# Kernel tuning notes

Hardware: AMD Instinct MI355X
Metric: run time of the kernel (lower is better)

Reference implementation:

```python
import jax, jax.numpy as jnp
import numpy as np
import math

D_MODEL = 1024
N_HEADS = 16
D_K = D_MODEL // N_HEADS
B, S = 4, 1024
MAX_REL = 64  # table built for 2*64-1 positions, clamped beyond


def setup_inputs() -> dict:
    key = jax.random.key(0)
    ks = jax.random.split(key, 11)
    init = 1.0 / math.sqrt(D_MODEL)
    def lin(k):
        kw, kb = jax.random.split(k)
        W = jax.random.uniform(kw, (D_MODEL, D_MODEL), jnp.float32, -init, init)
        b = jax.random.uniform(kb, (D_MODEL,), jnp.float32, -init, init)
        return W, b
    wq, bq = lin(ks[0]); wk, bk = lin(ks[1]); wv, bv = lin(ks[2]); wo, bo = lin(ks[3])
    x = jax.random.normal(ks[4], (B, S, D_MODEL), jnp.float32)
    rel_table = jax.random.normal(ks[5], (2 * MAX_REL - 1, N_HEADS), jnp.float32)
    mask = jnp.ones((B, 1, 1, S), jnp.int32)
    return {"x": x, "mask": mask, "wq": wq, "bq": bq, "wk": wk, "bk": bk,
            "wv": wv, "bv": bv, "wo": wo, "bo": bo, "rel_table": rel_table}


def reference(x, mask, wq, bq, wk, bk, wv, bv, wo, bo, rel_table):
    Bn, Sn, Dm = x.shape
    scale = math.sqrt(D_K)
    def heads(y):  # [B,S,D] -> [B,H,S,dk]
        return y.reshape(Bn, Sn, N_HEADS, D_K).transpose(0, 2, 1, 3)
    Q = heads(x @ wq.T + bq)
    K = heads(x @ wk.T + bk)
    V = heads(x @ wv.T + bv)
    scores = jnp.einsum('bhqd,bhkd->bhqk', Q, K) / scale
    # relative position bias gather, clamped to table range
    rel = jnp.arange(Sn)[None, :] - jnp.arange(Sn)[:, None] + MAX_REL - 1
    rel = jnp.clip(rel, 0, 2 * MAX_REL - 2)
    bias = rel_table[rel]                      # [S,S,H]
    scores = scores + bias.transpose(2, 0, 1)[None]  # [B,H,S,S]
    scores = jnp.where(mask == 0, jnp.float32(-1e9), scores)
    attn = jax.nn.softmax(scores, axis=-1)
    ctx = jnp.einsum('bhqk,bhkd->bhqd', attn, V)
    ctx = ctx.transpose(0, 2, 1, 3).reshape(Bn, Sn, Dm)
    return ctx @ wo.T + bo
```

## Files before the change

kernel.cpp:

```cpp
#include <hip/hip_runtime.h>
#include <hip/hip_bf16.h>

typedef __attribute__((ext_vector_type(8))) short short8;
typedef __attribute__((ext_vector_type(4))) short short4v;
typedef __attribute__((ext_vector_type(4))) float f32x4;

#define D_MODEL 1024
#define N_HEADS 16
#define D_KK 64
#define BATCH 4
#define SEQ 1024
#define NTOK (BATCH*SEQ)

#define LOG2E  1.44269504f
#define SCALE2 (0.125f * 1.44269504f)
#define NEGBIG (-1.44269504e9f)

#if __has_builtin(__builtin_amdgcn_mfma_f32_16x16x16bf16_1k)
#define HAVE_MFMA16 1
#else
#define HAVE_MFMA16 0
#endif

#if __has_builtin(__builtin_amdgcn_exp2f)
#define EXP2(x) __builtin_amdgcn_exp2f(x)
#else
#define EXP2(x) exp2f(x)
#endif

template<int N> struct ic { static constexpr int value = N; };

__device__ __forceinline__ short f2b(float f){
  unsigned u = __float_as_uint(f);
  u += 0x7fffu + ((u >> 16) & 1u);
  return (short)(u >> 16);
}

__device__ __forceinline__ void gl2lds16(const void* g, void* l){
  __builtin_amdgcn_global_load_lds(
      (const __attribute__((address_space(1))) void*)g,
      (__attribute__((address_space(3))) void*)l, 16, 0, 0);
}

__device__ __forceinline__ float max3f(float a, float b, float c){
  float d; asm("v_max3_f32 %0, %1, %2, %3" : "=v"(d) : "v"(a), "v"(b), "v"(c)); return d;
}
__device__ __forceinline__ float tmax16(const f32x4* sc){
  float t = max3f(sc[0][0], sc[0][1], sc[0][2]);
  t = max3f(t, sc[0][3], sc[1][0]);
  t = max3f(t, sc[1][1], sc[1][2]);
  t = max3f(t, sc[1][3], sc[2][0]);
  t = max3f(t, sc[2][1], sc[2][2]);
  t = max3f(t, sc[2][3], sc[3][0]);
  t = max3f(t, sc[3][1], sc[3][2]);
  return fmaxf(t, sc[3][3]);
}

__global__ __launch_bounds__(256) void cvt_all_kernel(
    const float* __restrict__ x,  const float* __restrict__ wq,
    const float* __restrict__ wk, const float* __restrict__ wv,
    const float* __restrict__ wo, short* __restrict__ dst)
{
  const size_t NX = (size_t)NTOK * D_MODEL;
  const size_t NW = (size_t)D_MODEL * D_MODEL;
  size_t e = ((size_t)blockIdx.x * 256 + threadIdx.x) * 4;
  const float* s;
  size_t off;
  if      (e < NX)        { s = x;  off = e; }
  else if (e < NX +   NW) { s = wq; off = e - NX; }
  else if (e < NX + 2*NW) { s = wk; off = e - NX -   NW; }
  else if (e < NX + 3*NW) { s = wv; off = e - NX - 2*NW; }
  else                    { s = wo; off = e - NX - 3*NW; }
  f32x4 v = *reinterpret_cast<const f32x4*>(s + off);
  short4v o;
  o[0]=f2b(v[0]); o[1]=f2b(v[1]); o[2]=f2b(v[2]); o[3]=f2b(v[3]);
  *reinterpret_cast<short4v*>(dst + e) = o;
}

template<int BN, int MODE, bool PRESC>
__device__ __forceinline__ void gemm_bt_body(const short* __restrict__ A,
    const short* __restrict__ W, const float* __restrict__ bias,
    void* __restrict__ Cout, int N, int K, int bm0, int bn0,
    short* AsB, short* BsB)
{
  constexpr int NF = BN / 32;
  const int tid = threadIdx.x, lane = tid & 63, w = tid >> 6;
  const int wr = w >> 1, wc = w & 1;
  const int srow = lane >> 3;
  const int scol = ((lane & 7) ^ srow) * 8;
  const int fr = lane & 15, g = lane >> 4;

  f32x4 acc[4][NF];
  #pragma unroll
  for (int m=0;m<4;m++)
    #pragma unroll
    for (int n=0;n<NF;n++) acc[m][n] = (f32x4){0.f,0.f,0.f,0.f};

  for (int k0 = 0; k0 < K; k0 += 64){
    __syncthreads();
    #pragma unroll
    for (int i=0;i<4;i++){
      const int c = w*4 + i;
      gl2lds16(A + (size_t)(bm0 + c*8 + srow)*K + k0 + scol, &AsB[c*8*64]);
    }
    #pragma unroll
    for (int i=0;i<NF;i++){
      const int c = w*NF + i;
      gl2lds16(W + (size_t)(bn0 + c*8 + srow)*K + k0 + scol, &BsB[c*8*64]);
    }
    __syncthreads();
    #pragma unroll
    for (int f=0; f<2; f++){
      short8 af[4], bfr[NF];
      #pragma unroll
      for (int m=0;m<4;m++){
        const int rr = wr*64 + m*16 + fr;
        af[m] = *reinterpret_cast<const short8*>(
            (const char*)AsB + rr*128 + ((g*16 + f*64) ^ ((rr&7)<<4)));
      }
      #pragma unroll
      for (int n=0;n<NF;n++){
        const int rr = wc*(BN/2) + n*16 + fr;
        bfr[n] = *reinterpret_cast<const short8*>(
            (const char*)BsB + rr*128 + ((g*16 + f*64) ^ ((rr&7)<<4)));
      }
      #pragma unroll
      for (int m=0;m<4;m++)
        #pragma unroll
        for (int n=0;n<NF;n++)
          acc[m][n] = __builtin_amdgcn_mfma_f32_16x16x32_bf16(af[m], bfr[n], acc[m][n], 0,0,0);
    }
  }

  #pragma unroll
  for (int n=0;n<NF;n++){
    const int col = bn0 + wc*(BN/2) + n*16 + fr;
    const float bv = bias[col];
    if (MODE == 2){
      const int hh = col >> 6, dd = col & 63;
      #pragma unroll
      for (int m=0;m<4;m++){
        const int row0 = bm0 + wr*64 + m*16 + g*4;
        const int bb = row0 >> 10, ss = row0 & 1023;
        short4v o;
        #pragma unroll
        for (int r=0;r<4;r++){
          float v = acc[m][n][r] + bv;
          if (PRESC) v *= SCALE2;
          o[r] = f2b(v);
        }
        *reinterpret_cast<short4v*>(
            (short*)Cout + ((size_t)(bb*N_HEADS+hh)*D_KK + dd)*SEQ + ss) = o;
      }
    } else {
      #pragma unroll
      for (int m=0;m<4;m++){
        const int row0 = bm0 + wr*64 + m*16 + g*4;
        #pragma unroll
        for (int r=0;r<4;r++){
          float v = acc[m][n][r] + bv;
          if (PRESC) v *= SCALE2;
          if (MODE == 1) ((float*)Cout)[(size_t)(row0+r)*N + col] = v;
          else           ((short*)Cout)[(size_t)(row0+r)*N + col] = f2b(v);
        }
      }
    }
  }
}

__global__ __launch_bounds__(256) void qkv_gemm_kernel(
    const short* __restrict__ X,
    const short* __restrict__ Wq, const short* __restrict__ Wk, const short* __restrict__ Wv,
    const float* __restrict__ bq, const float* __restrict__ bk, const float* __restrict__ bv,
    short* __restrict__ Q, short* __restrict__ K, short* __restrict__ V)
{
  __shared__ short As[128*64];
  __shared__ short Bs[64*64];
  const int bid = blockIdx.x;
  const int xcd = bid & 7, s = bid >> 3;
  const int z = s >> 6;
  const int rem = s & 63;
  const int bn0 = (rem >> 2) * 64;
  const int bm0 = (xcd * 4 + (rem & 3)) * 128;
  if (z == 0)      gemm_bt_body<64,0,true >(X, Wq, bq, Q, D_MODEL, D_MODEL, bm0, bn0, As, Bs);
  else if (z == 1) gemm_bt_body<64,0,false>(X, Wk, bk, K, D_MODEL, D_MODEL, bm0, bn0, As, Bs);
  else             gemm_bt_body<64,2,false>(X, Wv, bv, V, D_MODEL, D_MODEL, bm0, bn0, As, Bs);
}

__global__ __launch_bounds__(256) void out_gemm_kernel(
    const short* __restrict__ Ctx, const short* __restrict__ Wo,
    const float* __restrict__ bo, float* __restrict__ Out)
{
  __shared__ short As[128*64];
  __shared__ short Bs[64*64];
  const int bid = blockIdx.x;
  const int xcd = bid & 7, s = bid >> 3;
  const int bn0 = (s >> 2) * 64;
  const int bm0 = (xcd * 4 + (s & 3)) * 128;
  gemm_bt_body<64,1,false>(Ctx, Wo, bo, Out, D_MODEL, D_MODEL, bm0, bn0, As, Bs);
}

__global__ __launch_bounds__(512, 2) void attn_kernel(
    const short* __restrict__ Qb, const short* __restrict__ Kb,
    const short* __restrict__ Vtg, const int* __restrict__ mask,
    const float* __restrict__ rel_table, short* __restrict__ Ctx)
{
  const int bid = blockIdx.x;
  const int xcd = bid & 7, slot = bid >> 3;
  const int bh = xcd * 8 + (slot >> 3);
  const int qt = slot & 7;
  const int b = bh >> 4, h = bh & 15;
  const int q0 = qt * 128;
  const int tid = threadIdx.x, lane = tid & 63, w = tid >> 6;
  const int team = w >> 2, wt = w & 3;
  const int fr = lane & 15, g = lane >> 4;

  __shared__ short kvbuf[2][2][2][64][64];
  __shared__ float rel_pad[384];
  __shared__ float mb_all[2][8][64];
  __shared__ float ml[128][2];

  for (int i = tid; i < 384; i += 512){
    int d = i - 128;
    d = d < 0 ? 0 : (d > 126 ? 126 : d);
    rel_pad[i] = rel_table[d * N_HEADS + h] * LOG2E;
  }
  const float cb_lo = rel_table[0*N_HEADS + h]   * LOG2E;
  const float cb_hi = rel_table[126*N_HEADS + h] * LOG2E;

  for (int e = tid; e < 1024; e += 512){
    const int tm = e >> 9, tt = (e >> 6) & 7, i = e & 63;
    const int kvt = tm*512 + tt*64;
    const int delta = kvt - q0;
    const bool far = (delta <= -128 || delta >= 192);
    const float cb = far ? (delta > 0 ? cb_hi : cb_lo) : 0.f;
    mb_all[tm][tt][i] = mask[b*SEQ + kvt + i] ? cb : NEGBIG;
  }

  const short* Qg = Qb + (size_t)b*SEQ*D_MODEL + h*D_KK;
  const short* Kg = Kb + (size_t)b*SEQ*D_MODEL + h*D_KK;
  const short* Vg = Vtg + (size_t)bh*D_KK*SEQ;

  const int qa = q0 + wt*32 + fr;
  const int qb = qa + 16;
  short8 qfa[2], qfb[2];
  #pragma unroll
  for (int f=0; f<2; f++){
    qfa[f] = *reinterpret_cast<const short8*>(Qg + (size_t)qa*D_MODEL + g*8 + f*32);
    qfb[f] = *reinterpret_cast<const short8*>(Qg + (size_t)qb*D_MODEL + g*8 + f*32);
  }

  const char* lds0 = (const char*)kvbuf;
  const int swzb = (fr & 7) << 4;
  const char* kp[2];
  #pragma unroll
  for (int f=0; f<2; f++)
    kp[f] = lds0 + team*16384 + fr*128 + ((g*16 + f*64) ^ swzb);
  const char* vp[4];
  #pragma unroll
  for (int kt=0; kt<4; kt++)
    vp[kt] = lds0 + 32768 + team*16384 + fr*128
           + ((((kt*2 + (g>>1)) ^ (fr&7)) << 4) + (g&1)*8);
  const char* mbp0 = (const char*)mb_all + team*2048 + g*16;

  f32x4 ctxa[4], ctxb[4];
  #pragma unroll
  for (int dt=0; dt<4; dt++){ ctxa[dt] = (f32x4){0.f,0.f,0.f,0.f}; ctxb[dt] = ctxa[dt]; }
  float mruna = -3.0e38f, lruna = 0.f, mrunb = -3.0e38f, lrunb = 0.f;

  const int srow = lane >> 3;
  const int scol = ((lane & 7) ^ srow) * 8;
  auto stage = [&](int buf, int kv0){
    #pragma unroll
    for (int i=0;i<2;i++){
      const int c = wt*2 + i;
      gl2lds16(Kg + (size_t)(kv0 + c*8 + srow)*D_MODEL + scol, &kvbuf[0][team][buf][c*8][0]);
      gl2lds16(Vg + (size_t)(c*8 + srow)*SEQ + kv0 + scol,     &kvbuf[1][team][buf][c*8][0]);
    }
  };

  auto tile_step = [&](auto BUFC, auto VMC, int kv0, int tt) __attribute__((always_inline)) {
    constexpr int BUFL = decltype(BUFC)::value;
    constexpr int VM   = decltype(VMC)::value;

    if constexpr (VM == 4) asm volatile("s_waitcnt vmcnt(4)" ::: "memory");
    else                   asm volatile("s_waitcnt vmcnt(0)" ::: "memory");
    __builtin_amdgcn_s_barrier();
    asm volatile("" ::: "memory");

    const char* mbp = mbp0 + tt*256;

    f32x4 sca[4], scb[4];
    const int delta = kv0 - q0;
    if (delta <= -128 || delta >= 192){
      #pragma unroll
      for (int kt=0;kt<4;kt++){
        f32x4 mb4 = *reinterpret_cast<const f32x4*>(mbp + kt*64);
        sca[kt] = mb4;
        scb[kt] = mb4;
      }
    } else {
      const int pbase = delta + 63 - (wt*32 + fr) + 128 + g*4;
      f32x4 rr[5];
      #pragma unroll
      for (int j=0;j<5;j++)
        #pragma unroll
        for (int r=0;r<4;r++)
          rr[j][r] = rel_pad[pbase - 16 + j*16 + r];
      #pragma unroll
      for (int kt=0;kt<4;kt++){
        f32x4 mb4 = *reinterpret_cast<const f32x4*>(mbp + kt*64);
        #pragma unroll
        for (int r=0;r<4;r++){
          sca[kt][r] = rr[kt+1][r] + mb4[r];
          scb[kt][r] = rr[kt][r]   + mb4[r];
        }
      }
    }

    __builtin_amdgcn_s_setprio(1);
    #pragma unroll
    for (int kt=0;kt<4;kt++){
      #pragma unroll
      for (int f=0;f<2;f++){
        short8 kf = *reinterpret_cast<const short8*>(kp[f] + (kt*2048 + BUFL*8192));
        sca[kt] = __builtin_amdgcn_mfma_f32_16x16x32_bf16(kf, qfa[f], sca[kt], 0,0,0);
        scb[kt] = __builtin_amdgcn_mfma_f32_16x16x32_bf16(kf, qfb[f], scb[kt], 0,0,0);
      }
    }
    __builtin_amdgcn_s_setprio(0);

    short4v paa[4], pab[4];
    {
      const float tmax = tmax16(sca);
      if (!__all(tmax <= mruna + 8.f)){
        float tm = fmaxf(tmax, __shfl_xor(tmax, 16));
        tm = fmaxf(tm, __shfl_xor(tm, 32));
        const float mnew = fmaxf(mruna, tm);
        const float corr = EXP2(mruna - mnew);
        lruna *= corr;
        #pragma unroll
        for (int dt=0;dt<4;dt++)
          #pragma unroll
          for (int r=0;r<4;r++) ctxa[dt][r] *= corr;
        mruna = mnew;
      }
      float psum = 0.f;
      #pragma unroll
      for (int kt=0;kt<4;kt++){
        float p0 = EXP2(sca[kt][0] - mruna);
        float p1 = EXP2(sca[kt][1] - mruna);
        float p2 = EXP2(sca[kt][2] - mruna);
        float p3 = EXP2(sca[kt][3] - mruna);
        psum += (p0 + p1) + (p2 + p3);
        union { short4v s; __hip_bfloat162 hh[2]; } u;
        u.hh[0] = __float22bfloat162_rn(make_float2(p0, p1));
        u.hh[1] = __float22bfloat162_rn(make_float2(p2, p3));
        paa[kt] = u.s;
      }
      lruna += psum;
    }
    {
      const float tmax = tmax16(scb);
      if (!__all(tmax <= mrunb + 8.f)){
        float tm = fmaxf(tmax, __shfl_xor(tmax, 16));
        tm = fmaxf(tm, __shfl_xor(tm, 32));
        const float mnew = fmaxf(mrunb, tm);
        const float corr = EXP2(mrunb - mnew);
        lrunb *= corr;
        #pragma unroll
        for (int dt=0;dt<4;dt++)
          #pragma unroll
          for (int r=0;r<4;r++) ctxb[dt][r] *= corr;
        mrunb = mnew;
      }
      float psum = 0.f;
      #pragma unroll
      for (int kt=0;kt<4;kt++){
        float p0 = EXP2(scb[kt][0] - mrunb);
        float p1 = EXP2(scb[kt][1] - mrunb);
        float p2 = EXP2(scb[kt][2] - mrunb);
        float p3 = EXP2(scb[kt][3] - mrunb);
        psum += (p0 + p1) + (p2 + p3);
        union { short4v s; __hip_bfloat162 hh[2]; } u;
        u.hh[0] = __float22bfloat162_rn(make_float2(p0, p1));
        u.hh[1] = __float22bfloat162_rn(make_float2(p2, p3));
        pab[kt] = u.s;
      }
      lrunb += psum;
    }

    __builtin_amdgcn_s_setprio(1);
#if HAVE_MFMA16
    #pragma unroll
    for (int dt=0;dt<4;dt++){
      #pragma unroll
      for (int kt=0;kt<4;kt++){
        short4v va = *reinterpret_cast<const short4v*>(vp[kt] + (dt*2048 + BUFL*8192));
        ctxa[dt] = __builtin_amdgcn_mfma_f32_16x16x16bf16_1k(va, paa[kt], ctxa[dt], 0,0,0);
        ctxb[dt] = __builtin_amdgcn_mfma_f32_16x16x16bf16_1k(va, pab[kt], ctxb[dt], 0,0,0);
      }
    }
#else
    const char* vsb = lds0 + 32768 + team*16384 + BUFL*8192;
    #pragma unroll
    for (int f=0;f<2;f++){
      union { short8 s8; unsigned u[4]; } bfa, bfb;
      #pragma unroll
      for (int m=0;m<4;m++){
        const int srcl = ((g&1)*2 + (m>>1))*16 + fr;
        union { short4v s; unsigned u[2]; } ca0, ca1, cb0, cb1;
        ca0.s = paa[f*2+0]; ca1.s = paa[f*2+1];
        cb0.s = pab[f*2+0]; cb1.s = pab[f*2+1];
        unsigned a0 = __shfl((int)ca0.u[m&1], srcl);
        unsigned a1 = __shfl((int)ca1.u[m&1], srcl);
        bfa.u[m] = (g >> 1) ? a1 : a0;
        unsigned b0 = __shfl((int)cb0.u[m&1], srcl);
        unsigned b1 = __shfl((int)cb1.u[m&1], srcl);
        bfb.u[m] = (g >> 1) ? b1 : b0;
      }
      #pragma unroll
      for (int dt=0;dt<4;dt++){
        const int dr = dt*16 + fr;
        const int vswz = (dr & 7) << 4;
        short8 va = *reinterpret_cast<const short8*>(
            vsb + dr*128 + ((g*16 + f*64) ^ vswz));
        ctxa[dt] = __builtin_amdgcn_mfma_f32_16x16x32_bf16(va, bfa.s8, ctxa[dt], 0,0,0);
        ctxb[dt] = __builtin_amdgcn_mfma_f32_16x16x32_bf16(va, bfb.s8, ctxb[dt], 0,0,0);
      }
    }
#endif
    __builtin_amdgcn_s_setprio(0);

    asm volatile("" ::: "memory");
    __builtin_amdgcn_s_barrier();
  };

  const int kvbase = team * 512;
  __syncthreads();
  stage(0, kvbase);
  stage(1, kvbase + 64);

  for (int t = 0; t < 6; t += 2){
    tile_step(ic<0>{}, ic<4>{}, kvbase + t*64,     t);
    stage(0, kvbase + (t+2)*64);
    tile_step(ic<1>{}, ic<4>{}, kvbase + (t+1)*64, t+1);
    stage(1, kvbase + (t+3)*64);
  }
  tile_step(ic<0>{}, ic<4>{}, kvbase + 6*64, 6);
  tile_step(ic<1>{}, ic<0>{}, kvbase + 7*64, 7);
  asm volatile("" ::: "memory");

  lruna += __shfl_xor(lruna, 16);
  lruna += __shfl_xor(lruna, 32);
  lrunb += __shfl_xor(lrunb, 16);
  lrunb += __shfl_xor(lrunb, 32);

  float* mctx = (float*)&kvbuf[0][0][0][0][0];
  const int rowA = wt*32 + fr, rowB = rowA + 16;
  if (team == 1){
    #pragma unroll
    for (int dt=0;dt<4;dt++){
      *reinterpret_cast<f32x4*>(&mctx[rowA*72 + dt*16 + g*4]) = ctxa[dt];
      *reinterpret_cast<f32x4*>(&mctx[rowB*72 + dt*16 + g*4]) = ctxb[dt];
    }
    ml[rowA][0] = mruna; ml[rowA][1] = lruna;
    ml[rowB][0] = mrunb; ml[rowB][1] = lrunb;
  }
  __syncthreads();
  if (team == 0){
    {
      const float m1 = ml[rowA][0], l1 = ml[rowA][1];
      const float m  = fmaxf(mruna, m1);
      const float s0 = EXP2(mruna - m), s1 = EXP2(m1 - m);
      const float rl = 1.f / (lruna*s0 + l1*s1);
      #pragma unroll
      for (int dt=0;dt<4;dt++){
        f32x4 c1 = *reinterpret_cast<const f32x4*>(&mctx[rowA*72 + dt*16 + g*4]);
        short4v o;
        #pragma unroll
        for (int r=0;r<4;r++) o[r] = f2b((ctxa[dt][r]*s0 + c1[r]*s1) * rl);
        *reinterpret_cast<short4v*>(
            Ctx + (size_t)(b*SEQ + qa)*D_MODEL + h*D_KK + dt*16 + g*4) = o;
      }
    }
    {
      const float m1 = ml[rowB][0], l1 = ml[rowB][1];
      const float m  = fmaxf(mrunb, m1);
      const float s0 = EXP2(mrunb - m), s1 = EXP2(m1 - m);
      const float rl = 1.f / (lrunb*s0 + l1*s1);
      #pragma unroll
      for (int dt=0;dt<4;dt++){
        f32x4 c1 = *reinterpret_cast<const f32x4*>(&mctx[rowB*72 + dt*16 + g*4]);
        short4v o;
        #pragma unroll
        for (int r=0;r<4;r++) o[r] = f2b((ctxb[dt][r]*s0 + c1[r]*s1) * rl);
        *reinterpret_cast<short4v*>(
            Ctx + (size_t)(b*SEQ + qb)*D_MODEL + h*D_KK + dt*16 + g*4) = o;
      }
    }
  }
}

extern "C" void kernel_launch(void* const* d_in, const int* in_sizes, int n_in,
                              void* d_out, int out_size, void* d_ws, size_t ws_size,
                              hipStream_t stream) {
  const float* x    = (const float*)d_in[0];
  const int*   mask = (const int*)  d_in[1];
  const float* wq   = (const float*)d_in[2];
  const float* bq   = (const float*)d_in[3];
  const float* wk   = (const float*)d_in[4];
  const float* bk   = (const float*)d_in[5];
  const float* wv   = (const float*)d_in[6];
  const float* bv   = (const float*)d_in[7];
  const float* wo   = (const float*)d_in[8];
  const float* bo   = (const float*)d_in[9];
  const float* rel  = (const float*)d_in[10];

  const size_t NX = (size_t)NTOK * D_MODEL;
  const size_t NW = (size_t)D_MODEL * D_MODEL;
  if (ws_size < (NX + 4*NW + 4*NX) * sizeof(short)) return;
  short* xb   = (short*)d_ws;
  short* wqb  = xb  + NX;
  short* wkb  = wqb + NW;
  short* wvb  = wkb + NW;
  short* wob  = wvb + NW;
  short* Qb   = wob + NW;
  short* Kb   = Qb  + NX;
  short* Vtg  = Kb  + NX;
  short* Ctxb = Vtg + NX;

  cvt_all_kernel<<<8192, 256, 0, stream>>>(x, wq, wk, wv, wo, xb);

  qkv_gemm_kernel<<<1536, 256, 0, stream>>>(
      xb, wqb, wkb, wvb, bq, bk, bv, Qb, Kb, Vtg);

  attn_kernel<<<512, 512, 0, stream>>>(Qb, Kb, Vtg, mask, rel, Ctxb);

  out_gemm_kernel<<<512, 256, 0, stream>>>(Ctxb, wob, bo, (float*)d_out);
}
```

Measured before the change: 103.8 us.

## Fuse Q/K/V projections into one block sharing the X tile

The QKV GEMM kernel now computes the Q, K and V output tiles for the same row/column block inside one workgroup. It loads the X tile into LDS once per k-step and reuses it against three weight tiles, instead of launching separate blocks that each reload X. The grid shrinks from 1536 to 512 blocks. In exchange each block holds three times the accumulators and more LDS, which can lower occupancy and leaves fewer blocks to hide latency.

```diff
diff --git a/kernel.cpp b/kernel.cpp
--- a/kernel.cpp
+++ b/kernel.cpp
@@ -77,6 +77,109 @@
   *reinterpret_cast<short4v*>(dst + e) = o;
 }
 
+__global__ __launch_bounds__(256) void qkv_gemm_kernel(
+    const short* __restrict__ X,
+    const short* __restrict__ Wq, const short* __restrict__ Wk, const short* __restrict__ Wv,
+    const float* __restrict__ bq, const float* __restrict__ bk, const float* __restrict__ bv,
+    short* __restrict__ Q, short* __restrict__ K, short* __restrict__ V)
+{
+  __shared__ short As[128*64];
+  __shared__ short Bs[3][64*64];
+  const int bid = blockIdx.x;
+  const int xcd = bid & 7, s = bid >> 3;
+  const int bn0 = (s >> 2) * 64;
+  const int bm0 = (xcd * 4 + (s & 3)) * 128;
+
+  const int tid = threadIdx.x, lane = tid & 63, w = tid >> 6;
+  const int wr = w >> 1, wc = w & 1;
+  const int srow = lane >> 3;
+  const int scol = ((lane & 7) ^ srow) * 8;
+  const int fr = lane & 15, g = lane >> 4;
+
+  const short* const Wz[3] = {Wq, Wk, Wv};
+
+  f32x4 acc[3][4][2];
+  #pragma unroll
+  for (int z=0;z<3;z++)
+    #pragma unroll
+    for (int m=0;m<4;m++)
+      #pragma unroll
+      for (int n=0;n<2;n++) acc[z][m][n] = (f32x4){0.f,0.f,0.f,0.f};
+
+  for (int k0 = 0; k0 < D_MODEL; k0 += 64){
+    __syncthreads();
+    #pragma unroll
+    for (int i=0;i<4;i++){
+      const int c = w*4 + i;
+      gl2lds16(X + (size_t)(bm0 + c*8 + srow)*D_MODEL + k0 + scol, &As[c*8*64]);
+    }
+    #pragma unroll
+    for (int z=0;z<3;z++)
+      #pragma unroll
+      for (int i=0;i<2;i++){
+        const int c = w*2 + i;
+        gl2lds16(Wz[z] + (size_t)(bn0 + c*8 + srow)*D_MODEL + k0 + scol, &Bs[z][c*8*64]);
+      }
+    __syncthreads();
+    #pragma unroll
+    for (int f=0; f<2; f++){
+      short8 af[4];
+      #pragma unroll
+      for (int m=0;m<4;m++){
+        const int rr = wr*64 + m*16 + fr;
+        af[m] = *reinterpret_cast<const short8*>(
+            (const char*)As + rr*128 + ((g*16 + f*64) ^ ((rr&7)<<4)));
+      }
+      #pragma unroll
+      for (int z=0;z<3;z++){
+        short8 bfr[2];
+        #pragma unroll
+        for (int n=0;n<2;n++){
+          const int rr = wc*32 + n*16 + fr;
+          bfr[n] = *reinterpret_cast<const short8*>(
+              (const char*)&Bs[z][0] + rr*128 + ((g*16 + f*64) ^ ((rr&7)<<4)));
+        }
+        #pragma unroll
+        for (int m=0;m<4;m++)
+          #pragma unroll
+          for (int n=0;n<2;n++)
+            acc[z][m][n] = __builtin_amdgcn_mfma_f32_16x16x32_bf16(af[m], bfr[n], acc[z][m][n], 0,0,0);
+      }
+    }
+  }
+
+  #pragma unroll
+  for (int z=0;z<3;z++){
+    const float* bias = (z==0) ? bq : (z==1) ? bk : bv;
+    #pragma unroll
+    for (int n=0;n<2;n++){
+      const int col = bn0 + wc*32 + n*16 + fr;
+      const float bv_ = bias[col];
+      #pragma unroll
+      for (int m=0;m<4;m++){
+        const int row0 = bm0 + wr*64 + m*16 + g*4;
+        if (z == 2){
+          const int hh = col >> 6, dd = col & 63;
+          const int bb = row0 >> 10, ss = row0 & 1023;
+          short4v o;
+          #pragma unroll
+          for (int r=0;r<4;r++) o[r] = f2b(acc[z][m][n][r] + bv_);
+          *reinterpret_cast<short4v*>(
+              V + ((size_t)(bb*N_HEADS+hh)*D_KK + dd)*SEQ + ss) = o;
+        } else {
+          short* O = (z==0) ? Q : K;
+          #pragma unroll
+          for (int r=0;r<4;r++){
+            float v = acc[z][m][n][r] + bv_;
+            if (z == 0) v *= SCALE2;
+            O[(size_t)(row0+r)*D_MODEL + col] = f2b(v);
+          }
+        }
+      }
+    }
+  }
+}
+
 template<int BN, int MODE, bool PRESC>
 __device__ __forceinline__ void gemm_bt_body(const short* __restrict__ A,
     const short* __restrict__ W, const float* __restrict__ bias,
@@ -136,55 +239,18 @@
   for (int n=0;n<NF;n++){
     const int col = bn0 + wc*(BN/2) + n*16 + fr;
     const float bv = bias[col];
-    if (MODE == 2){
-      const int hh = col >> 6, dd = col & 63;
-      #pragma unroll
-      for (int m=0;m<4;m++){
-        const int row0 = bm0 + wr*64 + m*16 + g*4;
-        const int bb = row0 >> 10, ss = row0 & 1023;
-        short4v o;
-        #pragma unroll
-        for (int r=0;r<4;r++){
-          float v = acc[m][n][r] + bv;
-          if (PRESC) v *= SCALE2;
-          o[r] = f2b(v);
-        }
-        *reinterpret_cast<short4v*>(
-            (short*)Cout + ((size_t)(bb*N_HEADS+hh)*D_KK + dd)*SEQ + ss) = o;
-      }
-    } else {
-      #pragma unroll
-      for (int m=0;m<4;m++){
-        const int row0 = bm0 + wr*64 + m*16 + g*4;
-        #pragma unroll
-        for (int r=0;r<4;r++){
-          float v = acc[m][n][r] + bv;
-          if (PRESC) v *= SCALE2;
-          if (MODE == 1) ((float*)Cout)[(size_t)(row0+r)*N + col] = v;
-          else           ((short*)Cout)[(size_t)(row0+r)*N + col] = f2b(v);
-        }
-      }
-    }
-  }
-}
-
-__global__ __launch_bounds__(256) void qkv_gemm_kernel(
-    const short* __restrict__ X,
-    const short* __restrict__ Wq, const short* __restrict__ Wk, const short* __restrict__ Wv,
-    const float* __restrict__ bq, const float* __restrict__ bk, const float* __restrict__ bv,
-    short* __restrict__ Q, short* __restrict__ K, short* __restrict__ V)
-{
-  __shared__ short As[128*64];
-  __shared__ short Bs[64*64];
-  const int bid = blockIdx.x;
-  const int xcd = bid & 7, s = bid >> 3;
-  const int z = s >> 6;
-  const int rem = s & 63;
-  const int bn0 = (rem >> 2) * 64;
-  const int bm0 = (xcd * 4 + (rem & 3)) * 128;
-  if (z == 0)      gemm_bt_body<64,0,true >(X, Wq, bq, Q, D_MODEL, D_MODEL, bm0, bn0, As, Bs);
-  else if (z == 1) gemm_bt_body<64,0,false>(X, Wk, bk, K, D_MODEL, D_MODEL, bm0, bn0, As, Bs);
-  else             gemm_bt_body<64,2,false>(X, Wv, bv, V, D_MODEL, D_MODEL, bm0, bn0, As, Bs);
+    #pragma unroll
+    for (int m=0;m<4;m++){
+      const int row0 = bm0 + wr*64 + m*16 + g*4;
+      #pragma unroll
+      for (int r=0;r<4;r++){
+        float v = acc[m][n][r] + bv;
+        if (PRESC) v *= SCALE2;
+        if (MODE == 1) ((float*)Cout)[(size_t)(row0+r)*N + col] = v;
+        else           ((short*)Cout)[(size_t)(row0+r)*N + col] = f2b(v);
+      }
+    }
+  }
 }
 
 __global__ __launch_bounds__(256) void out_gemm_kernel(
@@ -532,7 +598,7 @@
 
   cvt_all_kernel<<<8192, 256, 0, stream>>>(x, wq, wk, wv, wo, xb);
 
-  qkv_gemm_kernel<<<1536, 256, 0, stream>>>(
+  qkv_gemm_kernel<<<512, 256, 0, stream>>>(
       xb, wqb, wkb, wvb, bq, bk, bv, Qb, Kb, Vtg);
 
   attn_kernel<<<512, 512, 0, stream>>>(Qb, Kb, Vtg, mask, rel, Ctxb);
```

Measured after the change: 100.3 us. 3.3% less time.
